# Kernel optimization log

Measured on AMD Instinct MI355X. Metric: run time of the kernel, lower is better.

## Reference

```python
import jax, jax.numpy as jnp
import numpy as np

B, N, F, H, L = 4, 512, 128, 4, 2
HID = 128            # edge MLP hidden width
LAM = 5.0            # sinkhorn_lambda
ITERS = 10           # sinkhorn_iter
NEG_SLOPE = 0.2      # GAT leaky-relu slope


def setup_inputs() -> dict:
    key = jax.random.key(0)
    ks = jax.random.split(key, 10)
    sc = 0.05
    return {
        "joint_features": jax.random.normal(ks[0], (B, N, F), jnp.float32),
        "joint_coords": jax.random.normal(ks[1], (B, N, 3), jnp.float32),
        # edge MLP: Linear(2F+1 -> 128), Linear(128 -> 1)
        "W1": jax.random.normal(ks[2], (2 * F + 1, HID), jnp.float32) * sc,
        "b1": jnp.zeros((HID,), jnp.float32),
        "W2": jax.random.normal(ks[3], (HID, 1), jnp.float32) * sc,
        "b2": jnp.zeros((1,), jnp.float32),
        # GAT layers (stacked over L): W (F -> H*F), attention vecs a_src/a_dst (H,F), bias (F)
        "Wg": jax.random.normal(ks[4], (L, F, H * F), jnp.float32) * sc,
        "a_src": jax.random.normal(ks[5], (L, H, F), jnp.float32) * sc,
        "a_dst": jax.random.normal(ks[6], (L, H, F), jnp.float32) * sc,
        "bg": jnp.zeros((L, F), jnp.float32),
    }


def _forward(joint_features, joint_coords, W1, b1, W2, b2, Wg, a_src, a_dst, bg):
    Bc, Nc, Fc = joint_features.shape
    # pairwise euclidean distances (B,N,N)  == torch.cdist(p=2)
    diff = joint_coords[:, :, None, :] - joint_coords[:, None, :, :]
    dist = jnp.sqrt(jnp.maximum(jnp.sum(diff * diff, axis=-1), 0.0))
    # edge MLP on cat([feat_i, feat_j, dist]). Fuse the concat by splitting W1
    # into row blocks: [W_a (F,HID); W_b (F,HID); w_d (HID,)] -- same math,
    # avoids materializing the (B,N,N,2F+1) concat tensor.
    Wa, Wb, wd = W1[:Fc], W1[Fc:2 * Fc], W1[2 * Fc]
    ha = joint_features @ Wa                      # (B,N,HID)
    hb = joint_features @ Wb                      # (B,N,HID)
    hidden = jax.nn.relu(ha[:, :, None, :] + hb[:, None, :, :]
                         + dist[..., None] * wd + b1)   # (B,N,N,HID)
    cost = jnp.squeeze(hidden @ W2, -1) + b2[0]         # (B,N,N)
    # Sinkhorn normalization: K = exp(-lambda * C), alternate row/col scaling
    def sink_step(P, _):
        P = P / jnp.sum(P, axis=-1, keepdims=True)
        P = P / jnp.sum(P, axis=-2, keepdims=True)
        return P, None
    adj, _ = jax.lax.scan(sink_step, jnp.exp(-LAM * cost), None, length=ITERS)
    # adj is strictly positive -> to_sparse() yields the fully-connected graph
    # per batch; GATConv(heads=H, concat=False) becomes dense attention over N.
    x = joint_features
    nlayers, nheads = Wg.shape[0], a_src.shape[1]
    for l in range(nlayers):
        xw = (x @ Wg[l]).reshape(Bc, Nc, nheads, Fc)            # (B,N,H,F)
        s_src = jnp.einsum('bnhf,hf->bnh', xw, a_src[l])        # sender score
        s_dst = jnp.einsum('bnhf,hf->bnh', xw, a_dst[l])        # receiver score
        # e[b,i,j,h]: message j -> i
        e = jax.nn.leaky_relu(s_dst[:, :, None, :] + s_src[:, None, :, :], NEG_SLOPE)
        attn = jax.nn.softmax(e, axis=2)                        # softmax over senders j
        x = jnp.einsum('bijh,bjhf->bihf', attn, xw).mean(axis=2) + bg[l]
    final_adj = jax.nn.sigmoid(jnp.einsum('bif,bjf->bij', x, x))
    return final_adj, adj


def reference(joint_features, joint_coords, W1, b1, W2, b2, Wg, a_src, a_dst, bg):
    return _forward(joint_features, joint_coords, W1, b1, W2, b2, Wg, a_src, a_dst, bg)
```

## Files before the change

### kernel.cpp

```cpp
#include <hip/hip_runtime.h>
#include <math.h>

#define NB 4
#define NN 512

__global__ void kA(const float* __restrict__ X, const float* __restrict__ W1,
                   const float* __restrict__ b1, float* __restrict__ ha,
                   float* __restrict__ hb, float* __restrict__ ru) {
  int b = blockIdx.y, n0 = blockIdx.x * 8;
  __shared__ float xs[8][128];
  int t = threadIdx.x;
  for (int q = t; q < 1024; q += 128) {
    int r = q >> 7, f = q & 127;
    xs[r][f] = X[(size_t)(b * NN + n0 + r) * 128 + f];
  }
  int flat = b * 64 + blockIdx.x;
  if (flat < 16) ru[flat * 128 + t] = 0.f;
  __syncthreads();
  float accA[8] = {0,0,0,0,0,0,0,0}, accB[8] = {0,0,0,0,0,0,0,0};
  for (int f = 0; f < 128; ++f) {
    float wa = W1[f * 128 + t];
    float wb = W1[(128 + f) * 128 + t];
#pragma unroll
    for (int r = 0; r < 8; ++r) {
      accA[r] = fmaf(xs[r][f], wa, accA[r]);
      accB[r] = fmaf(xs[r][f], wb, accB[r]);
    }
  }
  float b1v = b1[t];
#pragma unroll
  for (int r = 0; r < 8; ++r) {
    ha[(size_t)(b * NN + n0 + r) * 128 + t] = accA[r] + b1v;
    hb[(size_t)(b * NN + n0 + r) * 128 + t] = accB[r];
  }
}

__global__ void kB(const float* __restrict__ ha, const float* __restrict__ hb,
                   const float* __restrict__ coords, const float* __restrict__ W1,
                   const float* __restrict__ W2, const float* __restrict__ b2,
                   float* __restrict__ Km, float* __restrict__ ru) {
  int b = blockIdx.z, i0 = blockIdx.y * 32, j0 = blockIdx.x * 32;
  __shared__ alignas(16) float As[32][132];
  __shared__ alignas(16) float Bs[32][132];
  __shared__ alignas(16) float wd[128];
  __shared__ alignas(16) float w2[128];
  __shared__ float ci[32][3], cj[32][3];
  int t = threadIdx.x;
  for (int q = t; q < 1024; q += 256) {
    int r = q >> 5, c = (q & 31) * 4;
    *(float4*)&As[r][c] = *(const float4*)&ha[(size_t)(b * NN + i0 + r) * 128 + c];
    *(float4*)&Bs[r][c] = *(const float4*)&hb[(size_t)(b * NN + j0 + r) * 128 + c];
  }
  if (t < 128) { wd[t] = W1[256 * 128 + t]; w2[t] = W2[t]; }
  if (t < 96) ((float*)ci)[t] = coords[(size_t)(b * NN + i0) * 3 + t];
  else if (t < 192) ((float*)cj)[t - 96] = coords[(size_t)(b * NN + j0) * 3 + (t - 96)];
  __syncthreads();
  int tx = t & 15, ty = t >> 4;
  int ia = 2 * ty, ib = ia + 1, ja = tx, jb = tx + 16;
  float d00, d01, d10, d11;
  {
    float ax = ci[ia][0], ay = ci[ia][1], az = ci[ia][2];
    float bx = ci[ib][0], by = ci[ib][1], bz = ci[ib][2];
    float cx0 = cj[ja][0], cy0 = cj[ja][1], cz0 = cj[ja][2];
    float cx1 = cj[jb][0], cy1 = cj[jb][1], cz1 = cj[jb][2];
    float dx, dy, dz;
    dx = ax - cx0; dy = ay - cy0; dz = az - cz0;
    d00 = sqrtf(fmaxf(dx * dx + dy * dy + dz * dz, 0.f));
    dx = ax - cx1; dy = ay - cy1; dz = az - cz1;
    d01 = sqrtf(fmaxf(dx * dx + dy * dy + dz * dz, 0.f));
    dx = bx - cx0; dy = by - cy0; dz = bz - cz0;
    d10 = sqrtf(fmaxf(dx * dx + dy * dy + dz * dz, 0.f));
    dx = bx - cx1; dy = by - cy1; dz = bz - cz1;
    d11 = sqrtf(fmaxf(dx * dx + dy * dy + dz * dz, 0.f));
  }
  float a00 = 0, a01 = 0, a10 = 0, a11 = 0;
  for (int k = 0; k < 128; k += 4) {
    float4 A0 = *(float4*)&As[ia][k];
    float4 A1 = *(float4*)&As[ib][k];
    float4 B0 = *(float4*)&Bs[ja][k];
    float4 B1 = *(float4*)&Bs[jb][k];
    float4 W = *(float4*)&wd[k];
    float4 V = *(float4*)&w2[k];
#pragma unroll
    for (int kk = 0; kk < 4; ++kk) {
      float av = ((float*)&A0)[kk], av1 = ((float*)&A1)[kk];
      float bv = ((float*)&B0)[kk], bv1 = ((float*)&B1)[kk];
      float wv = ((float*)&W)[kk], vv = ((float*)&V)[kk];
      float t00 = fmaxf(fmaf(d00, wv, av + bv), 0.f);
      float t01 = fmaxf(fmaf(d01, wv, av + bv1), 0.f);
      float t10 = fmaxf(fmaf(d10, wv, av1 + bv), 0.f);
      float t11 = fmaxf(fmaf(d11, wv, av1 + bv1), 0.f);
      a00 = fmaf(t00, vv, a00);
      a01 = fmaf(t01, vv, a01);
      a10 = fmaf(t10, vv, a10);
      a11 = fmaf(t11, vv, a11);
    }
  }
  float b2v = b2[0];
  float k00 = __expf(-5.0f * (a00 + b2v));
  float k01 = __expf(-5.0f * (a01 + b2v));
  float k10 = __expf(-5.0f * (a10 + b2v));
  float k11 = __expf(-5.0f * (a11 + b2v));
  size_t r0 = (size_t)(b * NN + i0 + ia) * NN + j0;
  size_t r1 = (size_t)(b * NN + i0 + ib) * NN + j0;
  Km[r0 + ja] = k00; Km[r0 + jb] = k01;
  Km[r1 + ja] = k10; Km[r1 + jb] = k11;
  float s0 = k00 + k01, s1 = k10 + k11;
#pragma unroll
  for (int off = 1; off < 16; off <<= 1) {
    s0 += __shfl_xor(s0, off);
    s1 += __shfl_xor(s1, off);
  }
  if (tx == 0) {
    atomicAdd(&ru[b * NN + i0 + ia], s0);
    atomicAdd(&ru[b * NN + i0 + ib], s1);
  }
}


__device__ __forceinline__ void dCcol(const float* __restrict__ Km,
                                      const float* __restrict__ ru,
                                      float* __restrict__ rvp,
                                      float* sm, int ic, int b) {
  float* uinv = sm;
  int t = threadIdx.x;
  if (t < 32) uinv[t] = 1.0f / ru[b * NN + ic * 32 + t];
  __syncthreads();
  const float* Kp = Km + (size_t)(b * NN + ic * 32) * NN + t;
  float acc = 0.f;
#pragma unroll 8
  for (int ii = 0; ii < 32; ++ii) acc = fmaf(Kp[(size_t)ii * NN], uinv[ii], acc);
  rvp[ic * 2048 + b * NN + t] = acc;
}

__device__ __forceinline__ void dCrc(const float* __restrict__ Km,
                                     const float* __restrict__ rvpOld,
                                     float* __restrict__ rvpNew,
                                     float* __restrict__ ru,
                                     float* sm, int ic, int b) {
  float* vinv = sm;
  float* uinv = sm + 512;
  int t = threadIdx.x;
  {
    float s = 0.f;
#pragma unroll
    for (int q = 0; q < 16; ++q) s += rvpOld[q * 2048 + b * NN + t];
    vinv[t] = 1.0f / s;
  }
  __syncthreads();
  int w = t >> 6, l = t & 63;
#pragma unroll
  for (int m = 0; m < 4; ++m) {
    int r = ic * 32 + w * 4 + m;
    const float* Kp = Km + (size_t)(b * NN + r) * NN;
    float acc = 0.f;
#pragma unroll
    for (int mm = 0; mm < 8; ++mm) acc = fmaf(Kp[l + 64 * mm], vinv[l + 64 * mm], acc);
#pragma unroll
    for (int off = 1; off < 64; off <<= 1) acc += __shfl_xor(acc, off);
    if (l == 0) { uinv[w * 4 + m] = 1.0f / acc; ru[b * NN + r] = acc; }
  }
  __syncthreads();
  {
    const float* Kp = Km + (size_t)(b * NN + ic * 32) * NN + t;
    float acc = 0.f;
#pragma unroll 8
    for (int ii = 0; ii < 32; ++ii) acc = fmaf(Kp[(size_t)ii * NN], uinv[ii], acc);
    rvpNew[ic * 2048 + b * NN + t] = acc;
  }
}

__device__ __forceinline__ void dG1f(const float* __restrict__ x,
                                     const float* __restrict__ Wg,
                                     const float* __restrict__ asrc,
                                     const float* __restrict__ adst,
                                     float* __restrict__ xw,
                                     float* __restrict__ ssT,
                                     float* __restrict__ sdT,
                                     float* sm, int bx, int b) {
  int n0 = bx * 8;
  float* xs = sm;
  float* red = sm + 1024;
  int t = threadIdx.x;
  for (int q = t; q < 1024; q += 512)
    xs[q] = x[(size_t)(b * NN + n0 + (q >> 7)) * 128 + (q & 127)];
  __syncthreads();
  int c = t;
  float acc[8] = {0,0,0,0,0,0,0,0};
  for (int f = 0; f < 128; ++f) {
    float w0 = Wg[f * 512 + c];
#pragma unroll
    for (int r = 0; r < 8; ++r) acc[r] = fmaf(xs[r * 128 + f], w0, acc[r]);
  }
#pragma unroll
  for (int r = 0; r < 8; ++r)
    xw[(size_t)(b * NN + n0 + r) * 512 + c] = acc[r];
  float asv = asrc[c], adv = adst[c];
  int w = t >> 6, l = t & 63;
#pragma unroll
  for (int r = 0; r < 8; ++r) {
    float ps = acc[r] * asv, pd = acc[r] * adv;
#pragma unroll
    for (int off = 1; off < 64; off <<= 1) {
      ps += __shfl_xor(ps, off);
      pd += __shfl_xor(pd, off);
    }
    if (l == 0) { red[w * 16 + r * 2] = ps; red[w * 16 + r * 2 + 1] = pd; }
  }
  __syncthreads();
  if (t < 64) {
    int h = t >> 4, rr = t & 7, sd = (t >> 3) & 1;
    float s = red[(2 * h) * 16 + rr * 2 + sd] + red[(2 * h + 1) * 16 + rr * 2 + sd];
    float* dst = sd ? sdT : ssT;
    dst[(size_t)(b * 4 + h) * 512 + n0 + rr] = s;
  }
}

#define PLT 520
__device__ __forceinline__ void dG2t(const float* __restrict__ xw,
                                     const float* __restrict__ ssT,
                                     const float* __restrict__ sdT,
                                     float* __restrict__ partial,
                                     float* sm, int bx, int b) {
  int h = bx & 3, i0 = (bx >> 2) * 8;
  int bh = b * 4 + h;
  float* pls = sm;
  float* ssb = sm + 8192;
  float* sdl = sm + 8704;
  float* smaxsh = sm + 8712;
  float* mxl = sm + 8720;
  int t = threadIdx.x;
  {
    float v = ssT[(size_t)bh * 512 + t];
    ssb[t] = v;
#pragma unroll
    for (int off = 1; off < 64; off <<= 1) v = fmaxf(v, __shfl_xor(v, off));
    if ((t & 63) == 0) smaxsh[t >> 6] = v;
  }
  if (t < 8) sdl[t] = sdT[(size_t)bh * 512 + i0 + t];
  __syncthreads();
  if (t < 8) {
    float m = smaxsh[0];
#pragma unroll
    for (int q = 1; q < 8; ++q) m = fmaxf(m, smaxsh[q]);
    float mm = sdl[t] + m;
    mxl[t] = (mm >= 0.f) ? mm : 0.2f * mm;
  }
  __syncthreads();
  {
    int il = t >> 6, jq = t & 63;
    float mx = mxl[il], sdv = sdl[il];
    float pe[8];
    float den = 0.f;
#pragma unroll
    for (int jj = 0; jj < 8; ++jj) {
      int j = jj * 64 + jq;
      float e = sdv + ssb[j];
      e = (e >= 0.f) ? e : 0.2f * e;
      pe[jj] = __expf(e - mx);
      den += pe[jj];
    }
#pragma unroll
    for (int off = 1; off < 64; off <<= 1) den += __shfl_xor(den, off);
    float inv = 1.0f / (4.0f * den);
#pragma unroll
    for (int jj = 0; jj < 8; ++jj) pls[il * PLT + jj * 64 + jq] = pe[jj] * inv;
  }
  __syncthreads();
  int fq = t & 31, jh = t >> 5;
  const float* xp = xw + (size_t)(b * NN) * 512 + h * 128 + fq * 4;
  float4 acc[8];
#pragma unroll
  for (int r = 0; r < 8; ++r) acc[r] = make_float4(0.f, 0.f, 0.f, 0.f);
  int jbase = jh * 32;
#pragma unroll 4
  for (int jj = 0; jj < 32; ++jj) {
    int j = jbase + jj;
    float4 xv = *(const float4*)&xp[(size_t)j * 512];
#pragma unroll
    for (int r = 0; r < 8; ++r) {
      float p = pls[r * PLT + j];
      acc[r].x = fmaf(p, xv.x, acc[r].x);
      acc[r].y = fmaf(p, xv.y, acc[r].y);
      acc[r].z = fmaf(p, xv.z, acc[r].z);
      acc[r].w = fmaf(p, xv.w, acc[r].w);
    }
  }
  __syncthreads();
  int w = t >> 6;
#pragma unroll
  for (int r = 0; r < 8; ++r) {
    acc[r].x += __shfl_xor(acc[r].x, 32);
    acc[r].y += __shfl_xor(acc[r].y, 32);
    acc[r].z += __shfl_xor(acc[r].z, 32);
    acc[r].w += __shfl_xor(acc[r].w, 32);
  }
  float4* sc4 = (float4*)sm;
  if ((t & 63) < 32) {
#pragma unroll
    for (int r = 0; r < 8; ++r) sc4[w * 256 + r * 32 + fq] = acc[r];
  }
  __syncthreads();
  if (t < 256) {
    int r = t >> 5, ff = t & 31;
    float4 s = make_float4(0.f, 0.f, 0.f, 0.f);
#pragma unroll
    for (int q = 0; q < 8; ++q) {
      float4 u = sc4[q * 256 + r * 32 + ff];
      s.x += u.x; s.y += u.y; s.z += u.z; s.w += u.w;
    }
    *(float4*)&partial[((size_t)bh * NN + i0 + r) * 128 + ff * 4] = s;
  }
}

__device__ __forceinline__ void dRed(const float* __restrict__ partial,
                                     const float* __restrict__ bg,
                                     float* __restrict__ xo, int bx, int b) {
  int idx = bx * 512 + threadIdx.x;
  int f4 = idx & 31, i = idx >> 5;
  const float* pp = partial + (((size_t)b * 4) * NN + i) * 128 + f4 * 4;
  float4 s = *(const float4*)pp;
  const float* p1 = pp + (size_t)NN * 128;
  const float* p2 = pp + (size_t)2 * NN * 128;
  const float* p3 = pp + (size_t)3 * NN * 128;
  float4 v1 = *(const float4*)p1, v2 = *(const float4*)p2, v3 = *(const float4*)p3;
  float4 bb = *(const float4*)&bg[f4 * 4];
  s.x += v1.x + v2.x + v3.x + bb.x;
  s.y += v1.y + v2.y + v3.y + bb.y;
  s.z += v1.z + v2.z + v3.z + bb.z;
  s.w += v1.w + v2.w + v3.w + bb.w;
  *(float4*)&xo[(size_t)(b * NN + i) * 128 + f4 * 4] = s;
}

__device__ __forceinline__ void dF(const float* __restrict__ x,
                                   float* __restrict__ out,
                                   float* sm, int fid, int b) {
  int i0 = (fid >> 4) * 32, j0 = (fid & 15) * 32;
  float* As = sm;
  float* Bs = sm + 4224;
  int t = threadIdx.x;
  for (int q = t; q < 1024; q += 512) {
    int r = q >> 5, c = (q & 31) * 4;
    *(float4*)&As[r * 132 + c] = *(const float4*)&x[(size_t)(b * NN + i0 + r) * 128 + c];
    *(float4*)&Bs[r * 132 + c] = *(const float4*)&x[(size_t)(b * NN + j0 + r) * 128 + c];
  }
  __syncthreads();
  int tx = t & 31, ty = t >> 5;
  int ia = 2 * ty, ib = ia + 1;
  float a0 = 0.f, a1 = 0.f;
  for (int k = 0; k < 128; k += 4) {
    float4 A0 = *(float4*)&As[ia * 132 + k];
    float4 A1 = *(float4*)&As[ib * 132 + k];
    float4 B0 = *(float4*)&Bs[tx * 132 + k];
#pragma unroll
    for (int kk = 0; kk < 4; ++kk) {
      a0 = fmaf(((float*)&A0)[kk], ((float*)&B0)[kk], a0);
      a1 = fmaf(((float*)&A1)[kk], ((float*)&B0)[kk], a1);
    }
  }
  out[(size_t)(b * NN + i0 + ia) * NN + j0 + tx] = 1.0f / (1.0f + __expf(-a0));
  out[(size_t)(b * NN + i0 + ib) * NN + j0 + tx] = 1.0f / (1.0f + __expf(-a1));
}


__global__ __launch_bounds__(512) void nCcolG1f(
    const float* Km, const float* ru, float* rvpA,
    const float* X, const float* Wg, const float* as_, const float* ad_,
    float* xw, float* ssT, float* sdT) {
  __shared__ alignas(16) float sm[1280];
  if (blockIdx.x < 16) dCcol(Km, ru, rvpA, sm, blockIdx.x, blockIdx.y);
  else dG1f(X, Wg, as_, ad_, xw, ssT, sdT, sm, blockIdx.x - 16, blockIdx.y);
}

__global__ __launch_bounds__(512) void nCrcG2t(
    const float* Km, const float* rvpOld, float* rvpNew, float* ru,
    const float* xw, const float* ssT, const float* sdT, float* partial) {
  __shared__ alignas(16) float sm[8728];
  if (blockIdx.x < 16) dCrc(Km, rvpOld, rvpNew, ru, sm, blockIdx.x, blockIdx.y);
  else dG2t(xw, ssT, sdT, partial, sm, blockIdx.x - 16, blockIdx.y);
}

__global__ __launch_bounds__(512) void nCrcRed(
    const float* Km, const float* rvpOld, float* rvpNew, float* ru,
    const float* partial, const float* bg, float* xo) {
  __shared__ alignas(16) float sm[544];
  if (blockIdx.x < 16) dCrc(Km, rvpOld, rvpNew, ru, sm, blockIdx.x, blockIdx.y);
  else dRed(partial, bg, xo, blockIdx.x - 16, blockIdx.y);
}

__global__ __launch_bounds__(512) void nCrcG1f(
    const float* Km, const float* rvpOld, float* rvpNew, float* ru,
    const float* x, const float* Wg, const float* as_, const float* ad_,
    float* xw, float* ssT, float* sdT) {
  __shared__ alignas(16) float sm[1280];
  if (blockIdx.x < 16) dCrc(Km, rvpOld, rvpNew, ru, sm, blockIdx.x, blockIdx.y);
  else dG1f(x, Wg, as_, ad_, xw, ssT, sdT, sm, blockIdx.x - 16, blockIdx.y);
}

__global__ __launch_bounds__(512) void nCrcFp(
    const float* Km, const float* rvpOld, float* rvpNew, float* ru,
    const float* x, float* outF, int fbase) {
  __shared__ alignas(16) float sm[8448];
  if (blockIdx.x < 16) dCrc(Km, rvpOld, rvpNew, ru, sm, blockIdx.x, blockIdx.y);
  else dF(x, outF, sm, fbase + (blockIdx.x - 16), blockIdx.y);
}

__global__ __launch_bounds__(512) void kAdj(const float* __restrict__ Km,
                                            const float* __restrict__ ru,
                                            const float* __restrict__ rvp,
                                            float* __restrict__ out) {
  int rc = blockIdx.x, b = blockIdx.y;
  __shared__ float vinv[512];
  __shared__ float uinv[32];
  int t = threadIdx.x;
  {
    float s = 0.f;
#pragma unroll
    for (int ic = 0; ic < 16; ++ic) s += rvp[ic * 2048 + b * NN + t];
    vinv[t] = 1.0f / s;
  }
  if (t < 32) uinv[t] = 1.0f / ru[b * NN + rc * 32 + t];
  __syncthreads();
  float vj = vinv[t];
  const float* Kp = Km + (size_t)(b * NN + rc * 32) * NN + t;
  float* op = out + (size_t)(b * NN + rc * 32) * NN + t;
#pragma unroll 4
  for (int m = 0; m < 32; ++m) {
    op[(size_t)m * NN] = Kp[(size_t)m * NN] * uinv[m] * vj;
  }
}

extern "C" void kernel_launch(void* const* d_in, const int* in_sizes, int n_in,
                              void* d_out, int out_size, void* d_ws, size_t ws_size,
                              hipStream_t stream) {
  (void)in_sizes; (void)n_in; (void)out_size; (void)ws_size;
  const float* X   = (const float*)d_in[0];
  const float* C   = (const float*)d_in[1];
  const float* W1  = (const float*)d_in[2];
  const float* b1  = (const float*)d_in[3];
  const float* W2  = (const float*)d_in[4];
  const float* b2  = (const float*)d_in[5];
  const float* Wg  = (const float*)d_in[6];
  const float* as_ = (const float*)d_in[7];
  const float* ad_ = (const float*)d_in[8];
  const float* bg  = (const float*)d_in[9];
  float* out = (float*)d_out;
  float* ws = (float*)d_ws;

  float* ha    = ws;
  float* hb    = ws + 262144;
  float* Km    = ws + 524288;
  float* ru    = ws + 1572864;
  float* xw    = ws + 1591296;
  float* ssT   = ws + 2639872;
  float* sdT   = ws + 2648064;
  float* x1    = ws + 2656256;
  float* x2    = ws + 2918400;
  float* rvpA  = ws + 3180544;
  float* rvpB  = ws + 3246080;
  float* adj   = out + 1048576;
  float* partial = out;

  kA<<<dim3(64, 4), 128, 0, stream>>>(X, W1, b1, ha, hb, ru);
  kB<<<dim3(16, 16, 4), 256, 0, stream>>>(ha, hb, C, W1, W2, b2, Km, ru);
  nCcolG1f<<<dim3(80, 4), 512, 0, stream>>>(Km, ru, rvpA,
                                            X, Wg, as_, ad_, xw, ssT, sdT);
  nCrcG2t<<<dim3(272, 4), 512, 0, stream>>>(Km, rvpA, rvpB, ru,
                                            xw, ssT, sdT, partial);
  nCrcRed<<<dim3(48, 4), 512, 0, stream>>>(Km, rvpB, rvpA, ru,
                                           partial, bg, x1);
  nCrcG1f<<<dim3(80, 4), 512, 0, stream>>>(Km, rvpA, rvpB, ru,
                                           x1, Wg + 65536, as_ + 512, ad_ + 512,
                                           xw, ssT, sdT);
  nCrcG2t<<<dim3(272, 4), 512, 0, stream>>>(Km, rvpB, rvpA, ru,
                                            xw, ssT, sdT, partial);
  nCrcRed<<<dim3(48, 4), 512, 0, stream>>>(Km, rvpA, rvpB, ru,
                                           partial, bg + 128, x2);
  nCrcFp<<<dim3(80, 4), 512, 0, stream>>>(Km, rvpB, rvpA, ru, x2, out, 0);
  nCrcFp<<<dim3(80, 4), 512, 0, stream>>>(Km, rvpA, rvpB, ru, x2, out, 64);
  nCrcFp<<<dim3(80, 4), 512, 0, stream>>>(Km, rvpB, rvpA, ru, x2, out, 128);
  nCrcFp<<<dim3(80, 4), 512, 0, stream>>>(Km, rvpA, rvpB, ru, x2, out, 192);
  kAdj<<<dim3(16, 4), 512, 0, stream>>>(Km, ru, rvpB, adj);
}
```

Baseline: 162.0 us.

## Fuse edge-MLP kernel with first GAT projection and split attention over sender halves

Merges the edge-cost kernel and the layer-1 GAT projection into one launch, with a 256-thread projection variant, so the independent GAT work overlaps the cost-matrix construction. The first column-normalisation step becomes its own small kernel. The attention-aggregation blocks are split in two along the sender dimension, doubling the block count for better CU occupancy, and the reduction now sums eight partial slabs instead of four. This adds partial-buffer traffic and relies on the output region being large enough to hold the two slabs.

```diff
diff --git a/kernel.cpp b/kernel.cpp
--- a/kernel.cpp
+++ b/kernel.cpp
@@ -35,34 +35,41 @@
   }
 }
 
-__global__ void kB(const float* __restrict__ ha, const float* __restrict__ hb,
-                   const float* __restrict__ coords, const float* __restrict__ W1,
-                   const float* __restrict__ W2, const float* __restrict__ b2,
-                   float* __restrict__ Km, float* __restrict__ ru) {
-  int b = blockIdx.z, i0 = blockIdx.y * 32, j0 = blockIdx.x * 32;
-  __shared__ alignas(16) float As[32][132];
-  __shared__ alignas(16) float Bs[32][132];
-  __shared__ alignas(16) float wd[128];
-  __shared__ alignas(16) float w2[128];
-  __shared__ float ci[32][3], cj[32][3];
+
+__device__ __forceinline__ void dKb(const float* __restrict__ ha,
+                                    const float* __restrict__ hb,
+                                    const float* __restrict__ coords,
+                                    const float* __restrict__ W1,
+                                    const float* __restrict__ W2,
+                                    const float* __restrict__ b2,
+                                    float* __restrict__ Km,
+                                    float* __restrict__ ru,
+                                    float* sm, int jc, int ic, int b) {
+  float* As = sm;
+  float* Bs = sm + 4224;
+  float* wd = sm + 8448;
+  float* w2 = sm + 8576;
+  float* ci = sm + 8704;
+  float* cj = sm + 8800;
+  int i0 = ic * 32, j0 = jc * 32;
   int t = threadIdx.x;
   for (int q = t; q < 1024; q += 256) {
     int r = q >> 5, c = (q & 31) * 4;
-    *(float4*)&As[r][c] = *(const float4*)&ha[(size_t)(b * NN + i0 + r) * 128 + c];
-    *(float4*)&Bs[r][c] = *(const float4*)&hb[(size_t)(b * NN + j0 + r) * 128 + c];
+    *(float4*)&As[r * 132 + c] = *(const float4*)&ha[(size_t)(b * NN + i0 + r) * 128 + c];
+    *(float4*)&Bs[r * 132 + c] = *(const float4*)&hb[(size_t)(b * NN + j0 + r) * 128 + c];
   }
   if (t < 128) { wd[t] = W1[256 * 128 + t]; w2[t] = W2[t]; }
-  if (t < 96) ((float*)ci)[t] = coords[(size_t)(b * NN + i0) * 3 + t];
-  else if (t < 192) ((float*)cj)[t - 96] = coords[(size_t)(b * NN + j0) * 3 + (t - 96)];
+  if (t < 96) ci[t] = coords[(size_t)(b * NN + i0) * 3 + t];
+  else if (t < 192) cj[t - 96] = coords[(size_t)(b * NN + j0) * 3 + (t - 96)];
   __syncthreads();
   int tx = t & 15, ty = t >> 4;
   int ia = 2 * ty, ib = ia + 1, ja = tx, jb = tx + 16;
   float d00, d01, d10, d11;
   {
-    float ax = ci[ia][0], ay = ci[ia][1], az = ci[ia][2];
-    float bx = ci[ib][0], by = ci[ib][1], bz = ci[ib][2];
-    float cx0 = cj[ja][0], cy0 = cj[ja][1], cz0 = cj[ja][2];
-    float cx1 = cj[jb][0], cy1 = cj[jb][1], cz1 = cj[jb][2];
+    float ax = ci[ia * 3], ay = ci[ia * 3 + 1], az = ci[ia * 3 + 2];
+    float bx = ci[ib * 3], by = ci[ib * 3 + 1], bz = ci[ib * 3 + 2];
+    float cx0 = cj[ja * 3], cy0 = cj[ja * 3 + 1], cz0 = cj[ja * 3 + 2];
+    float cx1 = cj[jb * 3], cy1 = cj[jb * 3 + 1], cz1 = cj[jb * 3 + 2];
     float dx, dy, dz;
     dx = ax - cx0; dy = ay - cy0; dz = az - cz0;
     d00 = sqrtf(fmaxf(dx * dx + dy * dy + dz * dz, 0.f));
@@ -75,10 +82,10 @@
   }
   float a00 = 0, a01 = 0, a10 = 0, a11 = 0;
   for (int k = 0; k < 128; k += 4) {
-    float4 A0 = *(float4*)&As[ia][k];
-    float4 A1 = *(float4*)&As[ib][k];
-    float4 B0 = *(float4*)&Bs[ja][k];
-    float4 B1 = *(float4*)&Bs[jb][k];
+    float4 A0 = *(float4*)&As[ia * 132 + k];
+    float4 A1 = *(float4*)&As[ib * 132 + k];
+    float4 B0 = *(float4*)&Bs[ja * 132 + k];
+    float4 B1 = *(float4*)&Bs[jb * 132 + k];
     float4 W = *(float4*)&wd[k];
     float4 V = *(float4*)&w2[k];
 #pragma unroll
@@ -117,6 +124,66 @@
   }
 }
 
+__device__ __forceinline__ void dG1f256(const float* __restrict__ x,
+                                        const float* __restrict__ Wg,
+                                        const float* __restrict__ asrc,
+                                        const float* __restrict__ adst,
+                                        float* __restrict__ xw,
+                                        float* __restrict__ ssT,
+                                        float* __restrict__ sdT,
+                                        float* sm, int bx, int b) {
+  int n0 = bx * 8;
+  float* xs = sm;
+  float* red = sm + 1024;
+  int t = threadIdx.x;
+  for (int q = t; q < 1024; q += 256)
+    xs[q] = x[(size_t)(b * NN + n0 + (q >> 7)) * 128 + (q & 127)];
+  __syncthreads();
+  int c0 = t, c1 = t + 256;
+  float acc0[8] = {0,0,0,0,0,0,0,0}, acc1[8] = {0,0,0,0,0,0,0,0};
+  for (int f = 0; f < 128; ++f) {
+    float w0 = Wg[f * 512 + c0], w1 = Wg[f * 512 + c1];
+#pragma unroll
+    for (int r = 0; r < 8; ++r) {
+      float xv = xs[r * 128 + f];
+      acc0[r] = fmaf(xv, w0, acc0[r]);
+      acc1[r] = fmaf(xv, w1, acc1[r]);
+    }
+  }
+#pragma unroll
+  for (int r = 0; r < 8; ++r) {
+    xw[(size_t)(b * NN + n0 + r) * 512 + c0] = acc0[r];
+    xw[(size_t)(b * NN + n0 + r) * 512 + c1] = acc1[r];
+  }
+  float as0 = asrc[c0], ad0 = adst[c0];
+  float as1 = asrc[c1], ad1 = adst[c1];
+  int w = t >> 6, l = t & 63;
+#pragma unroll
+  for (int r = 0; r < 8; ++r) {
+    float ps0 = acc0[r] * as0, pd0 = acc0[r] * ad0;
+    float ps1 = acc1[r] * as1, pd1 = acc1[r] * ad1;
+#pragma unroll
+    for (int off = 1; off < 64; off <<= 1) {
+      ps0 += __shfl_xor(ps0, off);
+      pd0 += __shfl_xor(pd0, off);
+      ps1 += __shfl_xor(ps1, off);
+      pd1 += __shfl_xor(pd1, off);
+    }
+    if (l == 0) {
+      red[w * 32 + r * 4 + 0] = ps0; red[w * 32 + r * 4 + 1] = pd0;
+      red[w * 32 + r * 4 + 2] = ps1; red[w * 32 + r * 4 + 3] = pd1;
+    }
+  }
+  __syncthreads();
+  if (t < 64) {
+    int r = t & 7, h = (t >> 3) & 3, sd = t >> 5;
+    int wbase = (h & 1) ? 2 : 0;
+    int which = (h < 2 ? 0 : 2) + sd;
+    float s = red[wbase * 32 + r * 4 + which] + red[(wbase + 1) * 32 + r * 4 + which];
+    float* dst = sd ? sdT : ssT;
+    dst[(size_t)(b * 4 + h) * 512 + n0 + r] = s;
+  }
+}
 
 __device__ __forceinline__ void dCcol(const float* __restrict__ Km,
                                       const float* __restrict__ ru,
@@ -217,12 +284,12 @@
 }
 
 #define PLT 520
-__device__ __forceinline__ void dG2t(const float* __restrict__ xw,
-                                     const float* __restrict__ ssT,
-                                     const float* __restrict__ sdT,
-                                     float* __restrict__ partial,
-                                     float* sm, int bx, int b) {
-  int h = bx & 3, i0 = (bx >> 2) * 8;
+__device__ __forceinline__ void dG2tj(const float* __restrict__ xw,
+                                      const float* __restrict__ ssT,
+                                      const float* __restrict__ sdT,
+                                      float* __restrict__ partial,
+                                      float* sm, int bx, int b) {
+  int s = bx & 1, h = (bx >> 1) & 3, i0 = (bx >> 3) * 8;
   int bh = b * 4 + h;
   float* pls = sm;
   float* ssb = sm + 8192;
@@ -272,9 +339,9 @@
   float4 acc[8];
 #pragma unroll
   for (int r = 0; r < 8; ++r) acc[r] = make_float4(0.f, 0.f, 0.f, 0.f);
-  int jbase = jh * 32;
+  int jbase = s * 256 + jh * 16;
 #pragma unroll 4
-  for (int jj = 0; jj < 32; ++jj) {
+  for (int jj = 0; jj < 16; ++jj) {
     int j = jbase + jj;
     float4 xv = *(const float4*)&xp[(size_t)j * 512];
 #pragma unroll
@@ -303,32 +370,33 @@
   __syncthreads();
   if (t < 256) {
     int r = t >> 5, ff = t & 31;
-    float4 s = make_float4(0.f, 0.f, 0.f, 0.f);
+    float4 o = make_float4(0.f, 0.f, 0.f, 0.f);
 #pragma unroll
     for (int q = 0; q < 8; ++q) {
       float4 u = sc4[q * 256 + r * 32 + ff];
-      s.x += u.x; s.y += u.y; s.z += u.z; s.w += u.w;
-    }
-    *(float4*)&partial[((size_t)bh * NN + i0 + r) * 128 + ff * 4] = s;
-  }
-}
-
-__device__ __forceinline__ void dRed(const float* __restrict__ partial,
-                                     const float* __restrict__ bg,
-                                     float* __restrict__ xo, int bx, int b) {
+      o.x += u.x; o.y += u.y; o.z += u.z; o.w += u.w;
+    }
+    *(float4*)&partial[(size_t)s * 1048576 +
+                       ((size_t)bh * NN + i0 + r) * 128 + ff * 4] = o;
+  }
+}
+
+__device__ __forceinline__ void dRed8(const float* __restrict__ partial,
+                                      const float* __restrict__ bg,
+                                      float* __restrict__ xo, int bx, int b) {
   int idx = bx * 512 + threadIdx.x;
   int f4 = idx & 31, i = idx >> 5;
   const float* pp = partial + (((size_t)b * 4) * NN + i) * 128 + f4 * 4;
-  float4 s = *(const float4*)pp;
-  const float* p1 = pp + (size_t)NN * 128;
-  const float* p2 = pp + (size_t)2 * NN * 128;
-  const float* p3 = pp + (size_t)3 * NN * 128;
-  float4 v1 = *(const float4*)p1, v2 = *(const float4*)p2, v3 = *(const float4*)p3;
   float4 bb = *(const float4*)&bg[f4 * 4];
-  s.x += v1.x + v2.x + v3.x + bb.x;
-  s.y += v1.y + v2.y + v3.y + bb.y;
-  s.z += v1.z + v2.z + v3.z + bb.z;
-  s.w += v1.w + v2.w + v3.w + bb.w;
+  float4 s = bb;
+#pragma unroll
+  for (int sl = 0; sl < 2; ++sl) {
+#pragma unroll
+    for (int h = 0; h < 4; ++h) {
+      float4 v = *(const float4*)&pp[(size_t)sl * 1048576 + (size_t)h * NN * 128];
+      s.x += v.x; s.y += v.y; s.z += v.z; s.w += v.w;
+    }
+  }
   *(float4*)&xo[(size_t)(b * NN + i) * 128 + f4 * 4] = s;
 }
 
@@ -363,13 +431,23 @@
 }
 
 
-__global__ __launch_bounds__(512) void nCcolG1f(
-    const float* Km, const float* ru, float* rvpA,
+__global__ __launch_bounds__(256) void nKbG1f(
+    const float* ha, const float* hb, const float* C, const float* W1,
+    const float* W2, const float* b2, float* Km, float* ru,
     const float* X, const float* Wg, const float* as_, const float* ad_,
     float* xw, float* ssT, float* sdT) {
-  __shared__ alignas(16) float sm[1280];
-  if (blockIdx.x < 16) dCcol(Km, ru, rvpA, sm, blockIdx.x, blockIdx.y);
-  else dG1f(X, Wg, as_, ad_, xw, ssT, sdT, sm, blockIdx.x - 16, blockIdx.y);
+  __shared__ alignas(16) float sm[8896];
+  if (blockIdx.x < 256)
+    dKb(ha, hb, C, W1, W2, b2, Km, ru, sm, blockIdx.x & 15, blockIdx.x >> 4,
+        blockIdx.y);
+  else
+    dG1f256(X, Wg, as_, ad_, xw, ssT, sdT, sm, blockIdx.x - 256, blockIdx.y);
+}
+
+__global__ __launch_bounds__(512) void kCcol(
+    const float* Km, const float* ru, float* rvp) {
+  __shared__ float sm[32];
+  dCcol(Km, ru, rvp, sm, blockIdx.x, blockIdx.y);
 }
 
 __global__ __launch_bounds__(512) void nCrcG2t(
@@ -377,7 +455,7 @@
     const float* xw, const float* ssT, const float* sdT, float* partial) {
   __shared__ alignas(16) float sm[8728];
   if (blockIdx.x < 16) dCrc(Km, rvpOld, rvpNew, ru, sm, blockIdx.x, blockIdx.y);
-  else dG2t(xw, ssT, sdT, partial, sm, blockIdx.x - 16, blockIdx.y);
+  else dG2tj(xw, ssT, sdT, partial, sm, blockIdx.x - 16, blockIdx.y);
 }
 
 __global__ __launch_bounds__(512) void nCrcRed(
@@ -385,7 +463,7 @@
     const float* partial, const float* bg, float* xo) {
   __shared__ alignas(16) float sm[544];
   if (blockIdx.x < 16) dCrc(Km, rvpOld, rvpNew, ru, sm, blockIdx.x, blockIdx.y);
-  else dRed(partial, bg, xo, blockIdx.x - 16, blockIdx.y);
+  else dRed8(partial, bg, xo, blockIdx.x - 16, blockIdx.y);
 }
 
 __global__ __launch_bounds__(512) void nCrcG1f(
@@ -462,17 +540,17 @@
   float* partial = out;
 
   kA<<<dim3(64, 4), 128, 0, stream>>>(X, W1, b1, ha, hb, ru);
-  kB<<<dim3(16, 16, 4), 256, 0, stream>>>(ha, hb, C, W1, W2, b2, Km, ru);
-  nCcolG1f<<<dim3(80, 4), 512, 0, stream>>>(Km, ru, rvpA,
-                                            X, Wg, as_, ad_, xw, ssT, sdT);
-  nCrcG2t<<<dim3(272, 4), 512, 0, stream>>>(Km, rvpA, rvpB, ru,
+  nKbG1f<<<dim3(320, 4), 256, 0, stream>>>(ha, hb, C, W1, W2, b2, Km, ru,
+                                           X, Wg, as_, ad_, xw, ssT, sdT);
+  kCcol<<<dim3(16, 4), 512, 0, stream>>>(Km, ru, rvpA);
+  nCrcG2t<<<dim3(528, 4), 512, 0, stream>>>(Km, rvpA, rvpB, ru,
                                             xw, ssT, sdT, partial);
   nCrcRed<<<dim3(48, 4), 512, 0, stream>>>(Km, rvpB, rvpA, ru,
                                            partial, bg, x1);
   nCrcG1f<<<dim3(80, 4), 512, 0, stream>>>(Km, rvpA, rvpB, ru,
                                            x1, Wg + 65536, as_ + 512, ad_ + 512,
                                            xw, ssT, sdT);
-  nCrcG2t<<<dim3(272, 4), 512, 0, stream>>>(Km, rvpB, rvpA, ru,
+  nCrcG2t<<<dim3(528, 4), 512, 0, stream>>>(Km, rvpB, rvpA, ru,
                                             xw, ssT, sdT, partial);
   nCrcRed<<<dim3(48, 4), 512, 0, stream>>>(Km, rvpA, rvpB, ru,
                                            partial, bg + 128, x2);
```

After: 167.5 us. +3.4%, slower.
